# Kernel tuning notes

Hardware: AMD Instinct MI355X
Metric: run time of the kernel (lower is better)

## Reference

```python
import jax, jax.numpy as jnp
import numpy as np
from jax import lax

BIG = 1.0e6  # sentinel distance when a row contains no foreground pixel


def _dist1d(fg):
    """Exact 1D distance (in pixels) to nearest True along the last axis.

    fg: bool [..., W]. Returns float32 [..., W]; BIG where no True in the row.
    """
    W = fg.shape[-1]
    idx = jnp.arange(W, dtype=jnp.int32)
    # nearest foreground index to the left (inclusive)
    last = lax.cummax(jnp.where(fg, idx, -1), axis=fg.ndim - 1)
    d_left = jnp.where(last >= 0, (idx - last).astype(jnp.float32), BIG)
    # nearest foreground to the right: same scan on the reversed row
    fr = fg[..., ::-1]
    lastr = lax.cummax(jnp.where(fr, idx, -1), axis=fg.ndim - 1)
    d_right = jnp.where(lastr >= 0, (idx - lastr).astype(jnp.float32), BIG)[..., ::-1]
    return jnp.minimum(d_left, d_right)


def _edt2d(gt):
    """Exact Euclidean distance transform: distance from each pixel to the
    nearest gt==1 pixel (== scipy.distance_transform_edt(1-gt)).

    gt: [B, H, W] int. Returns float32 [B, H, W].
    Separable decomposition: D2(i,w) = min_j (d_row(j,w)^2 + (i-j)^2).
    """
    H = gt.shape[1]
    d_row = _dist1d(gt > 0)            # [B, H, W] 1D distances along rows
    dr2 = d_row * d_row                # squared row distances
    i = jnp.arange(H, dtype=jnp.float32)
    offs = (i[:, None] - i[None, :]) ** 2            # [Hi, Hj]
    # [B, Hi, Hj, W] = dr2 broadcast over i  +  (i-j)^2 broadcast over b, w
    d2 = jnp.min(dr2[:, None, :, :] + offs[None, :, :, None], axis=2)
    return jnp.sqrt(d2)


def setup_inputs() -> dict:
    key = jax.random.key(0)
    k1, k2 = jax.random.split(key)
    B, C, H, W = 8, 1, 256, 256
    logits = jax.random.normal(k1, (B, C, H, W), dtype=jnp.float32)
    target = jax.random.randint(k2, (B, C, H, W), 0, 2, dtype=jnp.int32)
    return {"logits": logits, "target": target}


def reference(logits, target):
    prob = jax.nn.sigmoid(logits)                      # [B, 1, H, W]
    D_gt = _edt2d(target[:, 0, :, :])[:, None, :, :]   # [B, 1, H, W]
    return jnp.mean(prob * D_gt)
```

## Files before the change

kernel.cpp:

```cpp
#include <hip/hip_runtime.h>


#define BIGF 1000000.0f
#define BIG2 (BIGF * BIGF)
#define BIGI (1 << 20)

constexpr int B = 8;
constexpr int H = 256;
constexpr int W = 256;
constexpr int NPIX = B * H * W;

__device__ __forceinline__ float block_reduce_sum_256(float v) {
    #pragma unroll
    for (int off = 32; off > 0; off >>= 1)
        v += __shfl_down(v, off, 64);
    __shared__ float s[4];
    const int lane = threadIdx.x & 63;
    const int wid  = threadIdx.x >> 6;
    if (lane == 0) s[wid] = v;
    __syncthreads();
    if (wid == 0) {
        v = (lane < 4) ? s[lane] : 0.0f;
        v += __shfl_down(v, 2, 64);
        v += __shfl_down(v, 1, 64);
    }
    return v;
}

__device__ __forceinline__ void upd16(const float4 m, float j0,
                                      float n0, float n1, float n2, float n3,
                                      float& b0, float& b1, float& b2, float& b3) {
    const float j1 = j0 + 1.0f, j2 = j0 + 2.0f, j3 = j0 + 3.0f;
    {
        const float c0 = fmaf(n0, j0, m.x), c1 = fmaf(n0, j1, m.y);
        const float c2 = fmaf(n0, j2, m.z), c3 = fmaf(n0, j3, m.w);
        b0 = fminf(b0, fminf(fminf(c0, c1), fminf(c2, c3)));
    }
    {
        const float c0 = fmaf(n1, j0, m.x), c1 = fmaf(n1, j1, m.y);
        const float c2 = fmaf(n1, j2, m.z), c3 = fmaf(n1, j3, m.w);
        b1 = fminf(b1, fminf(fminf(c0, c1), fminf(c2, c3)));
    }
    {
        const float c0 = fmaf(n2, j0, m.x), c1 = fmaf(n2, j1, m.y);
        const float c2 = fmaf(n2, j2, m.z), c3 = fmaf(n2, j3, m.w);
        b2 = fminf(b2, fminf(fminf(c0, c1), fminf(c2, c3)));
    }
    {
        const float c0 = fmaf(n3, j0, m.x), c1 = fmaf(n3, j1, m.y);
        const float c2 = fmaf(n3, j2, m.z), c3 = fmaf(n3, j3, m.w);
        b3 = fminf(b3, fminf(fminf(c0, c1), fminf(c2, c3)));
    }
}

__global__ __launch_bounds__(256) void row_dist_kernel(
        const int* __restrict__ target, float* __restrict__ dr2,
        unsigned* __restrict__ counter) {
    const int lane = threadIdx.x & 63;
    const int wv   = threadIdx.x >> 6;
    const int row  = (blockIdx.x << 2) + wv;

    if (blockIdx.x == 0 && threadIdx.x == 0) *counter = 0u;

    const int4 tv = *(const int4*)(target + row * W + (lane << 2));
    const int i0 = lane << 2;

    int lastL = -1;
    if (tv.x > 0) lastL = i0;
    if (tv.y > 0) lastL = i0 + 1;
    if (tv.z > 0) lastL = i0 + 2;
    if (tv.w > 0) lastL = i0 + 3;
    int incl = lastL;
    #pragma unroll
    for (int off = 1; off < 64; off <<= 1) {
        const int t = __shfl_up(incl, off, 64);
        if (lane >= off) incl = max(incl, t);
    }
    int runL = __shfl_up(incl, 1, 64);
    if (lane == 0) runL = -1;

    if (tv.x > 0) runL = i0;
    const int dl0 = (runL >= 0) ? (i0     - runL) : BIGI;
    if (tv.y > 0) runL = i0 + 1;
    const int dl1 = (runL >= 0) ? (i0 + 1 - runL) : BIGI;
    if (tv.z > 0) runL = i0 + 2;
    const int dl2 = (runL >= 0) ? (i0 + 2 - runL) : BIGI;
    if (tv.w > 0) runL = i0 + 3;
    const int dl3 = (runL >= 0) ? (i0 + 3 - runL) : BIGI;

    int nextR = BIGI;
    if (tv.w > 0) nextR = i0 + 3;
    if (tv.z > 0) nextR = i0 + 2;
    if (tv.y > 0) nextR = i0 + 1;
    if (tv.x > 0) nextR = i0;
    int inclR = nextR;
    #pragma unroll
    for (int off = 1; off < 64; off <<= 1) {
        const int t = __shfl_down(inclR, off, 64);
        if (lane < 64 - off) inclR = min(inclR, t);
    }
    int runR = __shfl_down(inclR, 1, 64);
    if (lane == 63) runR = BIGI;

    if (tv.w > 0) runR = i0 + 3;
    const int dR3 = runR - (i0 + 3);
    if (tv.z > 0) runR = i0 + 2;
    const int dR2v = runR - (i0 + 2);
    if (tv.y > 0) runR = i0 + 1;
    const int dR1 = runR - (i0 + 1);
    if (tv.x > 0) runR = i0;
    const int dR0 = runR - i0;

    const int d0 = min(dl0, dR0), d1 = min(dl1, dR1);
    const int d2 = min(dl2, dR2v), d3 = min(dl3, dR3);
    const float f0 = (float)d0, f1 = (float)d1, f2 = (float)d2, f3 = (float)d3;
    float4 o;
    o.x = (d0 > 255) ? BIG2 : f0 * f0;
    o.y = (d1 > 255) ? BIG2 : f1 * f1;
    o.z = (d2 > 255) ? BIG2 : f2 * f2;
    o.w = (d3 > 255) ? BIG2 : f3 * f3;
    *(float4*)(dr2 + row * W + (lane << 2)) = o;
}

__global__ __launch_bounds__(256) void col_pass_kernel(
        const float* __restrict__ logits, const float* __restrict__ dr2,
        float* __restrict__ partials, unsigned* __restrict__ counter,
        float* __restrict__ out) {
    __shared__ float s_q[4][256];
    const int t  = threadIdx.x;
    const int b  = blockIdx.x >> 6;
    const int w0 = (blockIdx.x & 63) << 2;

    const float4 v  = *(const float4*)(dr2 + (b * H + t) * W + w0);
    const float fj  = (float)t;
    const float fj2 = fj * fj;
    s_q[0][t] = fj2 + v.x;
    s_q[1][t] = fj2 + v.y;
    s_q[2][t] = fj2 + v.z;
    s_q[3][t] = fj2 + v.w;
    __syncthreads();

    const int lane = t & 63;
    const int wv   = t >> 6;
    const float i0f = (float)lane,         i1f = (float)(lane + 64);
    const float i2f = (float)(lane + 128), i3f = (float)(lane + 192);
    const float n0 = -2.0f * i0f, n1 = -2.0f * i1f;
    const float n2 = -2.0f * i2f, n3 = -2.0f * i3f;
    float b0 = 4e12f, b1 = 4e12f, b2 = 4e12f, b3 = 4e12f;

    float fjv = 0.0f;
    #pragma unroll 4
    for (int jv = 0; jv < 64; ++jv, fjv += 4.0f) {
        const float4 m = *(const float4*)&s_q[wv][jv << 2];
        upd16(m, fjv, n0, n1, n2, n3, b0, b1, b2, b3);
    }

    const int wcol = w0 + wv;
    const int base = (b * H + lane) * W + wcol;
    float acc;
    {
        const float dist = sqrtf(fmaf(i0f, i0f, b0));
        const float x = logits[base];
        acc = dist / (1.0f + expf(-x));
    }
    {
        const float dist = sqrtf(fmaf(i1f, i1f, b1));
        const float x = logits[base + 64 * W];
        acc += dist / (1.0f + expf(-x));
    }
    {
        const float dist = sqrtf(fmaf(i2f, i2f, b2));
        const float x = logits[base + 128 * W];
        acc += dist / (1.0f + expf(-x));
    }
    {
        const float dist = sqrtf(fmaf(i3f, i3f, b3));
        const float x = logits[base + 192 * W];
        acc += dist / (1.0f + expf(-x));
    }

    const float s = block_reduce_sum_256(acc);

    __shared__ bool amLast;
    if (t == 0) {
        partials[blockIdx.x] = s;
        __threadfence();
        const unsigned prev = atomicAdd(counter, 1u);
        amLast = (prev == gridDim.x - 1);
    }
    __syncthreads();
    if (amLast) {
        __threadfence();
        float fv = __hip_atomic_load(&partials[t], __ATOMIC_RELAXED,
                                     __HIP_MEMORY_SCOPE_AGENT);
        fv += __hip_atomic_load(&partials[t + 256], __ATOMIC_RELAXED,
                                __HIP_MEMORY_SCOPE_AGENT);
        __syncthreads();
        const float tot = block_reduce_sum_256(fv);
        if (t == 0) out[0] = tot * (1.0f / (float)NPIX);
    }
}

extern "C" void kernel_launch(void* const* d_in, const int* in_sizes, int n_in,
                              void* d_out, int out_size, void* d_ws, size_t ws_size,
                              hipStream_t stream) {
    const float* logits = (const float*)d_in[0];
    const int*   target = (const int*)d_in[1];

    float*    dr2      = (float*)d_ws;
    float*    partials = dr2 + NPIX;
    unsigned* counter  = (unsigned*)(partials + 512);

    row_dist_kernel<<<B * H / 4, 256, 0, stream>>>(target, dr2, counter);
    col_pass_kernel<<<B * W / 4, 256, 0, stream>>>(logits, dr2, partials,
                                                   counter, (float*)d_out);
}
```

Baseline: 80.66 us.

## Fuse row and column passes into one cooperative kernel with grid syncs

Merges the row-distance kernel and the column min-plus kernel into a single cooperative launch of 512 blocks, with grid.sync() between the phases and again before the final reduction. This drops one kernel launch and the atomic counter used to elect the last block. In exchange it pays for two grid-wide barriers, and the grid must fit co-resident, which the launch_bounds occupancy hint is meant to help with.

```diff
diff --git a/kernel.cpp b/kernel.cpp
--- a/kernel.cpp
+++ b/kernel.cpp
@@ -1,4 +1,7 @@
 #include <hip/hip_runtime.h>
+#include <hip/hip_cooperative_groups.h>
+
+namespace cg = cooperative_groups;
 
 
 #define BIGF 1000000.0f
@@ -9,6 +12,7 @@
 constexpr int H = 256;
 constexpr int W = 256;
 constexpr int NPIX = B * H * W;
+constexpr int NBLK = 512;
 
 __device__ __forceinline__ float block_reduce_sum_256(float v) {
     #pragma unroll
@@ -53,149 +57,139 @@
     }
 }
 
-__global__ __launch_bounds__(256) void row_dist_kernel(
-        const int* __restrict__ target, float* __restrict__ dr2,
-        unsigned* __restrict__ counter) {
-    const int lane = threadIdx.x & 63;
-    const int wv   = threadIdx.x >> 6;
-    const int row  = (blockIdx.x << 2) + wv;
-
-    if (blockIdx.x == 0 && threadIdx.x == 0) *counter = 0u;
-
-    const int4 tv = *(const int4*)(target + row * W + (lane << 2));
-    const int i0 = lane << 2;
-
-    int lastL = -1;
-    if (tv.x > 0) lastL = i0;
-    if (tv.y > 0) lastL = i0 + 1;
-    if (tv.z > 0) lastL = i0 + 2;
-    if (tv.w > 0) lastL = i0 + 3;
-    int incl = lastL;
-    #pragma unroll
-    for (int off = 1; off < 64; off <<= 1) {
-        const int t = __shfl_up(incl, off, 64);
-        if (lane >= off) incl = max(incl, t);
-    }
-    int runL = __shfl_up(incl, 1, 64);
-    if (lane == 0) runL = -1;
-
-    if (tv.x > 0) runL = i0;
-    const int dl0 = (runL >= 0) ? (i0     - runL) : BIGI;
-    if (tv.y > 0) runL = i0 + 1;
-    const int dl1 = (runL >= 0) ? (i0 + 1 - runL) : BIGI;
-    if (tv.z > 0) runL = i0 + 2;
-    const int dl2 = (runL >= 0) ? (i0 + 2 - runL) : BIGI;
-    if (tv.w > 0) runL = i0 + 3;
-    const int dl3 = (runL >= 0) ? (i0 + 3 - runL) : BIGI;
-
-    int nextR = BIGI;
-    if (tv.w > 0) nextR = i0 + 3;
-    if (tv.z > 0) nextR = i0 + 2;
-    if (tv.y > 0) nextR = i0 + 1;
-    if (tv.x > 0) nextR = i0;
-    int inclR = nextR;
-    #pragma unroll
-    for (int off = 1; off < 64; off <<= 1) {
-        const int t = __shfl_down(inclR, off, 64);
-        if (lane < 64 - off) inclR = min(inclR, t);
-    }
-    int runR = __shfl_down(inclR, 1, 64);
-    if (lane == 63) runR = BIGI;
-
-    if (tv.w > 0) runR = i0 + 3;
-    const int dR3 = runR - (i0 + 3);
-    if (tv.z > 0) runR = i0 + 2;
-    const int dR2v = runR - (i0 + 2);
-    if (tv.y > 0) runR = i0 + 1;
-    const int dR1 = runR - (i0 + 1);
-    if (tv.x > 0) runR = i0;
-    const int dR0 = runR - i0;
-
-    const int d0 = min(dl0, dR0), d1 = min(dl1, dR1);
-    const int d2 = min(dl2, dR2v), d3 = min(dl3, dR3);
-    const float f0 = (float)d0, f1 = (float)d1, f2 = (float)d2, f3 = (float)d3;
-    float4 o;
-    o.x = (d0 > 255) ? BIG2 : f0 * f0;
-    o.y = (d1 > 255) ? BIG2 : f1 * f1;
-    o.z = (d2 > 255) ? BIG2 : f2 * f2;
-    o.w = (d3 > 255) ? BIG2 : f3 * f3;
-    *(float4*)(dr2 + row * W + (lane << 2)) = o;
-}
-
-__global__ __launch_bounds__(256) void col_pass_kernel(
-        const float* __restrict__ logits, const float* __restrict__ dr2,
-        float* __restrict__ partials, unsigned* __restrict__ counter,
+__global__ __launch_bounds__(256, 2) void fused_kernel(
+        const float* __restrict__ logits, const int* __restrict__ target,
+        float* __restrict__ dr2, float* __restrict__ partials,
         float* __restrict__ out) {
-    __shared__ float s_q[4][256];
-    const int t  = threadIdx.x;
-    const int b  = blockIdx.x >> 6;
-    const int w0 = (blockIdx.x & 63) << 2;
-
-    const float4 v  = *(const float4*)(dr2 + (b * H + t) * W + w0);
-    const float fj  = (float)t;
-    const float fj2 = fj * fj;
-    s_q[0][t] = fj2 + v.x;
-    s_q[1][t] = fj2 + v.y;
-    s_q[2][t] = fj2 + v.z;
-    s_q[3][t] = fj2 + v.w;
-    __syncthreads();
-
+    cg::grid_group grid = cg::this_grid();
+    const int t    = threadIdx.x;
     const int lane = t & 63;
     const int wv   = t >> 6;
-    const float i0f = (float)lane,         i1f = (float)(lane + 64);
-    const float i2f = (float)(lane + 128), i3f = (float)(lane + 192);
-    const float n0 = -2.0f * i0f, n1 = -2.0f * i1f;
-    const float n2 = -2.0f * i2f, n3 = -2.0f * i3f;
-    float b0 = 4e12f, b1 = 4e12f, b2 = 4e12f, b3 = 4e12f;
-
-    float fjv = 0.0f;
-    #pragma unroll 4
-    for (int jv = 0; jv < 64; ++jv, fjv += 4.0f) {
-        const float4 m = *(const float4*)&s_q[wv][jv << 2];
-        upd16(m, fjv, n0, n1, n2, n3, b0, b1, b2, b3);
-    }
-
-    const int wcol = w0 + wv;
-    const int base = (b * H + lane) * W + wcol;
-    float acc;
-    {
-        const float dist = sqrtf(fmaf(i0f, i0f, b0));
-        const float x = logits[base];
-        acc = dist / (1.0f + expf(-x));
-    }
-    {
-        const float dist = sqrtf(fmaf(i1f, i1f, b1));
-        const float x = logits[base + 64 * W];
-        acc += dist / (1.0f + expf(-x));
-    }
-    {
-        const float dist = sqrtf(fmaf(i2f, i2f, b2));
-        const float x = logits[base + 128 * W];
-        acc += dist / (1.0f + expf(-x));
-    }
-    {
-        const float dist = sqrtf(fmaf(i3f, i3f, b3));
-        const float x = logits[base + 192 * W];
-        acc += dist / (1.0f + expf(-x));
-    }
-
-    const float s = block_reduce_sum_256(acc);
-
-    __shared__ bool amLast;
-    if (t == 0) {
-        partials[blockIdx.x] = s;
-        __threadfence();
-        const unsigned prev = atomicAdd(counter, 1u);
-        amLast = (prev == gridDim.x - 1);
-    }
-    __syncthreads();
-    if (amLast) {
-        __threadfence();
-        float fv = __hip_atomic_load(&partials[t], __ATOMIC_RELAXED,
-                                     __HIP_MEMORY_SCOPE_AGENT);
-        fv += __hip_atomic_load(&partials[t + 256], __ATOMIC_RELAXED,
-                                __HIP_MEMORY_SCOPE_AGENT);
+
+    {
+        const int row = (blockIdx.x << 2) + wv;
+        const int4 tv = *(const int4*)(target + row * W + (lane << 2));
+        const int i0 = lane << 2;
+
+        int lastL = -1;
+        if (tv.x > 0) lastL = i0;
+        if (tv.y > 0) lastL = i0 + 1;
+        if (tv.z > 0) lastL = i0 + 2;
+        if (tv.w > 0) lastL = i0 + 3;
+        int incl = lastL;
+        #pragma unroll
+        for (int off = 1; off < 64; off <<= 1) {
+            const int x = __shfl_up(incl, off, 64);
+            if (lane >= off) incl = max(incl, x);
+        }
+        int runL = __shfl_up(incl, 1, 64);
+        if (lane == 0) runL = -1;
+
+        if (tv.x > 0) runL = i0;
+        const int dl0 = (runL >= 0) ? (i0     - runL) : BIGI;
+        if (tv.y > 0) runL = i0 + 1;
+        const int dl1 = (runL >= 0) ? (i0 + 1 - runL) : BIGI;
+        if (tv.z > 0) runL = i0 + 2;
+        const int dl2 = (runL >= 0) ? (i0 + 2 - runL) : BIGI;
+        if (tv.w > 0) runL = i0 + 3;
+        const int dl3 = (runL >= 0) ? (i0 + 3 - runL) : BIGI;
+
+        int nextR = BIGI;
+        if (tv.w > 0) nextR = i0 + 3;
+        if (tv.z > 0) nextR = i0 + 2;
+        if (tv.y > 0) nextR = i0 + 1;
+        if (tv.x > 0) nextR = i0;
+        int inclR = nextR;
+        #pragma unroll
+        for (int off = 1; off < 64; off <<= 1) {
+            const int x = __shfl_down(inclR, off, 64);
+            if (lane < 64 - off) inclR = min(inclR, x);
+        }
+        int runR = __shfl_down(inclR, 1, 64);
+        if (lane == 63) runR = BIGI;
+
+        if (tv.w > 0) runR = i0 + 3;
+        const int dR3 = runR - (i0 + 3);
+        if (tv.z > 0) runR = i0 + 2;
+        const int dR2v = runR - (i0 + 2);
+        if (tv.y > 0) runR = i0 + 1;
+        const int dR1 = runR - (i0 + 1);
+        if (tv.x > 0) runR = i0;
+        const int dR0 = runR - i0;
+
+        const int d0 = min(dl0, dR0), d1 = min(dl1, dR1);
+        const int d2 = min(dl2, dR2v), d3 = min(dl3, dR3);
+        const float f0 = (float)d0, f1 = (float)d1;
+        const float f2 = (float)d2, f3 = (float)d3;
+        float4 o;
+        o.x = (d0 > 255) ? BIG2 : f0 * f0;
+        o.y = (d1 > 255) ? BIG2 : f1 * f1;
+        o.z = (d2 > 255) ? BIG2 : f2 * f2;
+        o.w = (d3 > 255) ? BIG2 : f3 * f3;
+        *(float4*)(dr2 + row * W + (lane << 2)) = o;
+    }
+
+    grid.sync();
+
+    __shared__ float s_q[4][256];
+    {
+        const int b  = blockIdx.x >> 6;
+        const int w0 = (blockIdx.x & 63) << 2;
+
+        const float4 v  = *(const float4*)(dr2 + (b * H + t) * W + w0);
+        const float fj  = (float)t;
+        const float fj2 = fj * fj;
+        s_q[0][t] = fj2 + v.x;
+        s_q[1][t] = fj2 + v.y;
+        s_q[2][t] = fj2 + v.z;
+        s_q[3][t] = fj2 + v.w;
         __syncthreads();
+
+        const float i0f = (float)lane,         i1f = (float)(lane + 64);
+        const float i2f = (float)(lane + 128), i3f = (float)(lane + 192);
+        const float n0 = -2.0f * i0f, n1 = -2.0f * i1f;
+        const float n2 = -2.0f * i2f, n3 = -2.0f * i3f;
+        float b0 = 4e12f, b1 = 4e12f, b2 = 4e12f, b3 = 4e12f;
+
+        float fjv = 0.0f;
+        #pragma unroll 4
+        for (int jv = 0; jv < 64; ++jv, fjv += 4.0f) {
+            const float4 m = *(const float4*)&s_q[wv][jv << 2];
+            upd16(m, fjv, n0, n1, n2, n3, b0, b1, b2, b3);
+        }
+
+        const int wcol = w0 + wv;
+        const int base = (b * H + lane) * W + wcol;
+        float acc;
+        {
+            const float dist = sqrtf(fmaf(i0f, i0f, b0));
+            const float x = logits[base];
+            acc = dist / (1.0f + expf(-x));
+        }
+        {
+            const float dist = sqrtf(fmaf(i1f, i1f, b1));
+            const float x = logits[base + 64 * W];
+            acc += dist / (1.0f + expf(-x));
+        }
+        {
+            const float dist = sqrtf(fmaf(i2f, i2f, b2));
+            const float x = logits[base + 128 * W];
+            acc += dist / (1.0f + expf(-x));
+        }
+        {
+            const float dist = sqrtf(fmaf(i3f, i3f, b3));
+            const float x = logits[base + 192 * W];
+            acc += dist / (1.0f + expf(-x));
+        }
+
+        const float s = block_reduce_sum_256(acc);
+        if (t == 0) partials[blockIdx.x] = s;
+    }
+
+    grid.sync();
+
+    if (blockIdx.x == 0) {
+        float fv = partials[t] + partials[t + 256];
         const float tot = block_reduce_sum_256(fv);
         if (t == 0) out[0] = tot * (1.0f / (float)NPIX);
     }
@@ -207,11 +201,12 @@
     const float* logits = (const float*)d_in[0];
     const int*   target = (const int*)d_in[1];
 
-    float*    dr2      = (float*)d_ws;
-    float*    partials = dr2 + NPIX;
-    unsigned* counter  = (unsigned*)(partials + 512);
-
-    row_dist_kernel<<<B * H / 4, 256, 0, stream>>>(target, dr2, counter);
-    col_pass_kernel<<<B * W / 4, 256, 0, stream>>>(logits, dr2, partials,
-                                                   counter, (float*)d_out);
-}
+    float* dr2      = (float*)d_ws;
+    float* partials = dr2 + NPIX;
+    float* outp     = (float*)d_out;
+
+    void* args[] = {(void*)&logits, (void*)&target, (void*)&dr2,
+                    (void*)&partials, (void*)&outp};
+    hipLaunchCooperativeKernel((const void*)fused_kernel, dim3(NBLK), dim3(256),
+                               args, 0, stream);
+}
```

After: 178.7 us. +121.6%, slower.
